# Kernel optimization log

Hardware: AMD Instinct MI355X
Metric: run time of the kernel (lower is better)

Reference implementation:

```python
import jax, jax.numpy as jnp
import numpy as np

N_E = 1024
E_DIM = 256
BETA = 0.25


def setup_inputs() -> dict:
    key = jax.random.key(0)
    k1, k2 = jax.random.split(key)
    z = jax.random.normal(k1, (16, E_DIM, 64, 64), dtype=jnp.float32)
    # nn.Embedding weight initialized uniform(-1/n_e, 1/n_e)
    codebook = jax.random.uniform(k2, (N_E, E_DIM), dtype=jnp.float32,
                                  minval=-1.0 / N_E, maxval=1.0 / N_E)
    return {"z": z, "codebook": codebook}


def reference(z, codebook):
    B, C, H, W = z.shape
    zp = jnp.transpose(z, (0, 2, 3, 1))              # [B,H,W,C]
    zf = zp.reshape(-1, C)                           # [N, e_dim]
    d = (jnp.sum(zf * zf, axis=1, keepdims=True)
         + jnp.sum(codebook * codebook, axis=1)
         - 2.0 * zf @ codebook.T)                    # [N, n_e]
    idx = jnp.argmin(d, axis=1)                      # [N]
    # one-hot @ codebook == direct gather
    z_q = codebook[idx].reshape(zp.shape)            # [B,H,W,C]

    e_latent_loss = jnp.mean((jax.lax.stop_gradient(z_q) - zp) ** 2)
    q_latent_loss = jnp.mean((z_q - jax.lax.stop_gradient(zp)) ** 2)
    codebook_loss = q_latent_loss + BETA * e_latent_loss

    # straight-through estimator
    z_q_st = zp + jax.lax.stop_gradient(z_q - zp)
    out = jnp.transpose(z_q_st, (0, 3, 1, 2))        # [B,C,H,W]
    indices = idx.reshape(B, 1, H, W)
    return out, codebook_loss, indices
```

## Files before the change

### kernel.cpp

```cpp
#include <hip/hip_runtime.h>

#define NB 16
#define NC 256
#define NH 64
#define NW 64
#define NK 1024
#define HW (NH * NW)
#define NPOS (NB * HW)
#define NOUT (NB * NC * HW)
#define NSLOT 256

__device__ __forceinline__ float sq_rn(float x) { return __fmul_rn(x, x); }

__device__ __forceinline__ float pairwise_sumsq_256(const float* __restrict__ a,
                                                    int stride) {
    float s_half[2];
#pragma unroll
    for (int h = 0; h < 2; ++h) {
        const float* base = a + (size_t)(h * 128) * stride;
        float r[8];
#pragma unroll
        for (int j = 0; j < 8; ++j) r[j] = sq_rn(base[(size_t)j * stride]);
        for (int i = 8; i < 128; i += 8) {
#pragma unroll
            for (int j = 0; j < 8; ++j)
                r[j] = __fadd_rn(r[j], sq_rn(base[(size_t)(i + j) * stride]));
        }
        s_half[h] = __fadd_rn(
            __fadd_rn(__fadd_rn(r[0], r[1]), __fadd_rn(r[2], r[3])),
            __fadd_rn(__fadd_rn(r[4], r[5]), __fadd_rn(r[6], r[7])));
    }
    return __fadd_rn(s_half[0], s_half[1]);
}

__global__ __launch_bounds__(256) void cnorm_kernel(const float* __restrict__ cb,
                                                    float* __restrict__ cnorm) {
    int k = blockIdx.x * 256 + threadIdx.x;
    if (k < NK) {
        cnorm[k] = pairwise_sumsq_256(cb + (size_t)k * NC, 1);
    }
}

__global__ __launch_bounds__(256) void transpose_cb_kernel(const float* __restrict__ cb,
                                                           float* __restrict__ cbT) {
    const int k = blockIdx.x;
    const int d = threadIdx.x;
    cbT[(size_t)d * NK + k] = cb[(size_t)k * NC + d];
}

__device__ __forceinline__ void pf4(float4* __restrict__ buf,
                                    const float* __restrict__ cp, int ds) {
#pragma unroll
    for (int q = 0; q < 8; ++q)
        buf[q] = *(const float4*)(cp + (size_t)(ds + (q >> 1)) * NK + (q & 1) * 4);
}

__device__ __forceinline__ void compute4(const float4* __restrict__ cbuf,
                                         float acc[8][8],
                                         const float (*z_lds)[64],
                                         int ds, int pg) {
#pragma unroll
    for (int dl = 0; dl < 4; ++dl) {
        const int d = ds + dl;
        const float4 za = *(const float4*)&z_lds[d][pg * 8];
        const float4 zb = *(const float4*)&z_lds[d][pg * 8 + 4];
        const float zf[8] = {za.x, za.y, za.z, za.w, zb.x, zb.y, zb.z, zb.w};
        const float4 ca = cbuf[dl * 2];
        const float4 cc = cbuf[dl * 2 + 1];
        const float cf[8] = {ca.x, ca.y, ca.z, ca.w, cc.x, cc.y, cc.z, cc.w};
#pragma unroll
        for (int i = 0; i < 8; ++i)
#pragma unroll
            for (int j = 0; j < 8; ++j)
                acc[i][j] = __fmaf_rn(zf[i], cf[j], acc[i][j]);
    }
}

__global__ __launch_bounds__(256, 2) void argmin_kernel(const float* __restrict__ z,
                                                        const float* __restrict__ cbT,
                                                        const float* __restrict__ cnorm,
                                                        int* __restrict__ idx_ws,
                                                        float* __restrict__ idx_out) {
    __shared__ float z_lds[256][64];
    __shared__ float znorm_s[64];
    __shared__ float red_v[4][64];
    __shared__ int   red_i[4][64];

    const int blk = blockIdx.x;
    const int b = blk >> 6;
    const int hw0 = (blk & 63) * 64;
    const int t = threadIdx.x;
    const int lane = t & 63;
    const int wave = t >> 6;
    const int pg = lane & 7;
    const int cg = lane >> 3;

    const float* zg = z + (size_t)b * (NC * HW) + hw0;

#pragma unroll 4
    for (int i = 0; i < 16; ++i) {
        const int flat4 = i * 1024 + t * 4;
        const int d = flat4 >> 6;
        const int p = flat4 & 63;
        const float4 v = *(const float4*)(zg + (size_t)d * HW + p);
        *(float4*)&z_lds[d][p] = v;
    }
    if (wave == 0) znorm_s[lane] = pairwise_sumsq_256(zg + lane, HW);
    __syncthreads();

    float zn[8];
#pragma unroll
    for (int i = 0; i < 8; ++i) zn[i] = znorm_s[pg * 8 + i];

    float best[8];
    int bid[8];
#pragma unroll
    for (int i = 0; i < 8; ++i) { best[i] = 3.4e38f; bid[i] = 0; }

#pragma unroll 1
    for (int pass = 0; pass < 4; ++pass) {
        float acc[8][8];
#pragma unroll
        for (int i = 0; i < 8; ++i)
#pragma unroll
            for (int j = 0; j < 8; ++j) acc[i][j] = 0.f;

        const int k0 = wave * 256 + pass * 64 + cg * 8;
        const float* cp = cbT + k0;

        float4 bufA[8], bufB[8];
        pf4(bufA, cp, 0);
#pragma unroll 1
        for (int it = 0; it < 32; ++it) {
            const int ds = it * 8;
            pf4(bufB, cp, ds + 4);
            compute4(bufA, acc, z_lds, ds, pg);
            if (ds + 8 < 256) pf4(bufA, cp, ds + 8);
            compute4(bufB, acc, z_lds, ds + 4, pg);
        }

        const float4 cn0 = *(const float4*)(cnorm + k0);
        const float4 cn1 = *(const float4*)(cnorm + k0 + 4);
        const float cnf[8] = {cn0.x, cn0.y, cn0.z, cn0.w, cn1.x, cn1.y, cn1.z, cn1.w};
#pragma unroll
        for (int j = 0; j < 8; ++j) {
            const int k = k0 + j;
#pragma unroll
            for (int i = 0; i < 8; ++i) {
                const float sc = __fsub_rn(__fadd_rn(zn[i], cnf[j]),
                                           __fmul_rn(2.0f, acc[i][j]));
                if (sc < best[i]) { best[i] = sc; bid[i] = k; }
            }
        }
    }

#pragma unroll
    for (int off = 32; off >= 8; off >>= 1) {
#pragma unroll
        for (int i = 0; i < 8; ++i) {
            const float v = __shfl_down(best[i], off, 64);
            const int d2 = __shfl_down(bid[i], off, 64);
            if (v < best[i] || (v == best[i] && d2 < bid[i])) {
                best[i] = v;
                bid[i] = d2;
            }
        }
    }
    if (cg == 0) {
#pragma unroll
        for (int i = 0; i < 8; ++i) {
            red_v[wave][pg * 8 + i] = best[i];
            red_i[wave][pg * 8 + i] = bid[i];
        }
    }
    __syncthreads();

    if (t < 64) {
        float bv = red_v[0][t];
        int bi = red_i[0][t];
#pragma unroll
        for (int w = 1; w < 4; ++w) {
            const float v = red_v[w][t];
            const int i2 = red_i[w][t];
            if (v < bv || (v == bv && i2 < bi)) { bv = v; bi = i2; }
        }
        const int g = b * HW + hw0 + t;
        idx_ws[g] = bi;
        idx_out[g] = (float)bi;
    }
}

__global__ __launch_bounds__(256) void gather_loss_kernel(const float* __restrict__ z,
                                                          const float* __restrict__ cb,
                                                          const int* __restrict__ idx_ws,
                                                          float* __restrict__ out,
                                                          double* __restrict__ loss_acc) {
    const unsigned g = blockIdx.x * 256u + threadIdx.x;
    const unsigned e = g * 4u;
    const unsigned w = e & 63u;
    const unsigned h = (e >> 6) & 63u;
    const unsigned c = (e >> 12) & 255u;
    const unsigned b = e >> 20;

    const unsigned p = b * HW + h * NW + w;

    const int4 iv = *(const int4*)(idx_ws + p);
    const float4 z4 = *(const float4*)(z + e);

    float4 o;
    o.x = cb[(size_t)iv.x * NC + c];
    o.y = cb[(size_t)iv.y * NC + c];
    o.z = cb[(size_t)iv.z * NC + c];
    o.w = cb[(size_t)iv.w * NC + c];

    *(float4*)(out + e) = o;

    const float d0 = o.x - z4.x;
    const float d1 = o.y - z4.y;
    const float d2 = o.z - z4.z;
    const float d3 = o.w - z4.w;
    float part = d0 * d0 + d1 * d1 + d2 * d2 + d3 * d3;

#pragma unroll
    for (int off = 32; off > 0; off >>= 1) part += __shfl_down(part, off, 64);

    __shared__ float wsum[4];
    const int lane = threadIdx.x & 63;
    const int wave = threadIdx.x >> 6;
    if (lane == 0) wsum[wave] = part;
    __syncthreads();
    if (threadIdx.x == 0) {
        float s = wsum[0] + wsum[1] + wsum[2] + wsum[3];
        atomicAdd(loss_acc + (blockIdx.x & (NSLOT - 1)), (double)s);
    }
}

__global__ void finalize_kernel(const double* __restrict__ loss_acc,
                                float* __restrict__ out_loss) {
    if (threadIdx.x == 0) {
        double s = 0.0;
        for (int i = 0; i < NSLOT; ++i) s += loss_acc[i];
        *out_loss = (float)(1.25 * s / (double)NOUT);
    }
}

extern "C" void kernel_launch(void* const* d_in, const int* in_sizes, int n_in,
                              void* d_out, int out_size, void* d_ws, size_t ws_size,
                              hipStream_t stream) {
    const float* z = (const float*)d_in[0];
    const float* cb = (const float*)d_in[1];

    float* out = (float*)d_out;
    float* loss_out = out + NOUT;
    float* idx_out = out + NOUT + 1;

    double* loss_acc = (double*)d_ws;
    float* cnorm = (float*)((char*)d_ws + 2048);
    int* idx_ws = (int*)((char*)d_ws + 2048 + 4096);
    float* cbT = (float*)((char*)d_ws + 2048 + 4096 + NPOS * 4);

    hipMemsetAsync(d_ws, 0, 2048, stream);
    cnorm_kernel<<<(NK + 255) / 256, 256, 0, stream>>>(cb, cnorm);
    transpose_cb_kernel<<<NK, 256, 0, stream>>>(cb, cbT);
    argmin_kernel<<<NPOS / 64, 256, 0, stream>>>(z, cbT, cnorm, idx_ws, idx_out);
    gather_loss_kernel<<<NOUT / 1024, 256, 0, stream>>>(z, cb, idx_ws, out, loss_acc);
    finalize_kernel<<<1, 64, 0, stream>>>(loss_acc, loss_out);
}
```

Before: 593.6 us.

## Use 512-thread argmin blocks with 8 waves and drop double-buffered codebook prefetch

The argmin kernel now runs 512 threads (8 waves) per block, each wave covering 128 codebook entries in 2 passes instead of 256 in 4, with launch bounds asking for 4 blocks per CU. The explicit A/B register double-buffering of codebook loads is replaced by a single per-iteration load, which lowers register pressure. Latency hiding now relies on more resident waves rather than software prefetch. The risk is more load stalls per wave if occupancy does not rise as intended, and LDS use per block (about 64KB of z) may cap how many blocks fit per CU.

After: 757.0 us. 1.28x slower.

```diff
diff --git a/kernel.cpp b/kernel.cpp
--- a/kernel.cpp
+++ b/kernel.cpp
@@ -48,43 +48,15 @@
     cbT[(size_t)d * NK + k] = cb[(size_t)k * NC + d];
 }
 
-__device__ __forceinline__ void pf4(float4* __restrict__ buf,
-                                    const float* __restrict__ cp, int ds) {
-#pragma unroll
-    for (int q = 0; q < 8; ++q)
-        buf[q] = *(const float4*)(cp + (size_t)(ds + (q >> 1)) * NK + (q & 1) * 4);
-}
-
-__device__ __forceinline__ void compute4(const float4* __restrict__ cbuf,
-                                         float acc[8][8],
-                                         const float (*z_lds)[64],
-                                         int ds, int pg) {
-#pragma unroll
-    for (int dl = 0; dl < 4; ++dl) {
-        const int d = ds + dl;
-        const float4 za = *(const float4*)&z_lds[d][pg * 8];
-        const float4 zb = *(const float4*)&z_lds[d][pg * 8 + 4];
-        const float zf[8] = {za.x, za.y, za.z, za.w, zb.x, zb.y, zb.z, zb.w};
-        const float4 ca = cbuf[dl * 2];
-        const float4 cc = cbuf[dl * 2 + 1];
-        const float cf[8] = {ca.x, ca.y, ca.z, ca.w, cc.x, cc.y, cc.z, cc.w};
-#pragma unroll
-        for (int i = 0; i < 8; ++i)
-#pragma unroll
-            for (int j = 0; j < 8; ++j)
-                acc[i][j] = __fmaf_rn(zf[i], cf[j], acc[i][j]);
-    }
-}
-
-__global__ __launch_bounds__(256, 2) void argmin_kernel(const float* __restrict__ z,
+__global__ __launch_bounds__(512, 4) void argmin_kernel(const float* __restrict__ z,
                                                         const float* __restrict__ cbT,
                                                         const float* __restrict__ cnorm,
                                                         int* __restrict__ idx_ws,
                                                         float* __restrict__ idx_out) {
     __shared__ float z_lds[256][64];
     __shared__ float znorm_s[64];
-    __shared__ float red_v[4][64];
-    __shared__ int   red_i[4][64];
+    __shared__ float red_v[8][64];
+    __shared__ int   red_i[8][64];
 
     const int blk = blockIdx.x;
     const int b = blk >> 6;
@@ -97,9 +69,9 @@
 
     const float* zg = z + (size_t)b * (NC * HW) + hw0;
 
-#pragma unroll 4
-    for (int i = 0; i < 16; ++i) {
-        const int flat4 = i * 1024 + t * 4;
+#pragma unroll
+    for (int i = 0; i < 8; ++i) {
+        const int flat4 = i * 2048 + t * 4;
         const int d = flat4 >> 6;
         const int p = flat4 & 63;
         const float4 v = *(const float4*)(zg + (size_t)d * HW + p);
@@ -108,46 +80,62 @@
     if (wave == 0) znorm_s[lane] = pairwise_sumsq_256(zg + lane, HW);
     __syncthreads();
 
-    float zn[8];
-#pragma unroll
-    for (int i = 0; i < 8; ++i) zn[i] = znorm_s[pg * 8 + i];
-
     float best[8];
     int bid[8];
 #pragma unroll
     for (int i = 0; i < 8; ++i) { best[i] = 3.4e38f; bid[i] = 0; }
 
 #pragma unroll 1
-    for (int pass = 0; pass < 4; ++pass) {
+    for (int pass = 0; pass < 2; ++pass) {
         float acc[8][8];
 #pragma unroll
         for (int i = 0; i < 8; ++i)
 #pragma unroll
             for (int j = 0; j < 8; ++j) acc[i][j] = 0.f;
 
-        const int k0 = wave * 256 + pass * 64 + cg * 8;
+        const int k0 = wave * 128 + pass * 64 + cg * 8;
         const float* cp = cbT + k0;
 
-        float4 bufA[8], bufB[8];
-        pf4(bufA, cp, 0);
 #pragma unroll 1
-        for (int it = 0; it < 32; ++it) {
-            const int ds = it * 8;
-            pf4(bufB, cp, ds + 4);
-            compute4(bufA, acc, z_lds, ds, pg);
-            if (ds + 8 < 256) pf4(bufA, cp, ds + 8);
-            compute4(bufB, acc, z_lds, ds + 4, pg);
+        for (int it = 0; it < 64; ++it) {
+            const int ds = it * 4;
+            float4 cbuf[8];
+#pragma unroll
+            for (int q = 0; q < 8; ++q)
+                cbuf[q] = *(const float4*)(cp + (size_t)(ds + (q >> 1)) * NK
+                                              + (q & 1) * 4);
+#pragma unroll
+            for (int dl = 0; dl < 4; ++dl) {
+                const int d = ds + dl;
+                const float4 za = *(const float4*)&z_lds[d][pg * 8];
+                const float4 zb = *(const float4*)&z_lds[d][pg * 8 + 4];
+                const float zf[8] = {za.x, za.y, za.z, za.w,
+                                     zb.x, zb.y, zb.z, zb.w};
+                const float4 ca = cbuf[dl * 2];
+                const float4 cc = cbuf[dl * 2 + 1];
+                const float cf[8] = {ca.x, ca.y, ca.z, ca.w,
+                                     cc.x, cc.y, cc.z, cc.w};
+#pragma unroll
+                for (int i = 0; i < 8; ++i)
+#pragma unroll
+                    for (int j = 0; j < 8; ++j)
+                        acc[i][j] = __fmaf_rn(zf[i], cf[j], acc[i][j]);
+            }
         }
 
         const float4 cn0 = *(const float4*)(cnorm + k0);
         const float4 cn1 = *(const float4*)(cnorm + k0 + 4);
-        const float cnf[8] = {cn0.x, cn0.y, cn0.z, cn0.w, cn1.x, cn1.y, cn1.z, cn1.w};
+        const float cnf[8] = {cn0.x, cn0.y, cn0.z, cn0.w,
+                              cn1.x, cn1.y, cn1.z, cn1.w};
+        float znl[8];
+#pragma unroll
+        for (int i = 0; i < 8; ++i) znl[i] = znorm_s[pg * 8 + i];
 #pragma unroll
         for (int j = 0; j < 8; ++j) {
             const int k = k0 + j;
 #pragma unroll
             for (int i = 0; i < 8; ++i) {
-                const float sc = __fsub_rn(__fadd_rn(zn[i], cnf[j]),
+                const float sc = __fsub_rn(__fadd_rn(znl[i], cnf[j]),
                                            __fmul_rn(2.0f, acc[i][j]));
                 if (sc < best[i]) { best[i] = sc; bid[i] = k; }
             }
@@ -179,7 +167,7 @@
         float bv = red_v[0][t];
         int bi = red_i[0][t];
 #pragma unroll
-        for (int w = 1; w < 4; ++w) {
+        for (int w = 1; w < 8; ++w) {
             const float v = red_v[w][t];
             const int i2 = red_i[w][t];
             if (v < bv || (v == bv && i2 < bi)) { bv = v; bi = i2; }
@@ -262,7 +250,7 @@
     hipMemsetAsync(d_ws, 0, 2048, stream);
     cnorm_kernel<<<(NK + 255) / 256, 256, 0, stream>>>(cb, cnorm);
     transpose_cb_kernel<<<NK, 256, 0, stream>>>(cb, cbT);
-    argmin_kernel<<<NPOS / 64, 256, 0, stream>>>(z, cbT, cnorm, idx_ws, idx_out);
+    argmin_kernel<<<NPOS / 64, 512, 0, stream>>>(z, cbT, cnorm, idx_ws, idx_out);
     gather_loss_kernel<<<NOUT / 1024, 256, 0, stream>>>(z, cb, idx_ws, out, loss_acc);
     finalize_kernel<<<1, 64, 0, stream>>>(loss_acc, loss_out);
 }
```
